# Kernel optimization log

Hardware: AMD Instinct MI355X
Metric: run time of the kernel (lower is better)

The kernel has to match this reference:

```python
import jax, jax.numpy as jnp
import numpy as np

T, B, H, D = 512, 64, 512, 32  # timesteps, batch, hidden_size, process_dim


def _softplus_beta(x, beta):
    # torch.nn.Softplus(beta): log(1+exp(beta*x))/beta
    return jax.nn.softplus(beta * x) / beta


def setup_inputs() -> dict:
    key = jax.random.key(0)
    ks = jax.random.split(key, 5)
    seq_dt = jax.random.uniform(ks[0], (T, B), jnp.float32)  # time until next event
    seq_types = jax.random.randint(ks[1], (T, B), 0, D)      # event type ids in [0, D)
    embed = jax.random.normal(ks[2], (D + 1, D), jnp.float32) * 0.1
    embed = embed.at[D].set(0.0)  # padding_idx row
    # 7 gate linears fused: order [input_g, forget_g, output_g, input_target, forget_target, z_gate, decay]
    W_gates = jax.random.normal(ks[3], (D + H, 7 * H), jnp.float32) * (1.0 / np.sqrt(D + H))
    b_gates = jax.random.normal(ks[4], (7 * H,), jnp.float32) * 0.05
    h0 = jnp.zeros((B, H), jnp.float32)
    c0 = jnp.zeros((B, H), jnp.float32)
    c_target0 = jnp.zeros((B, H), jnp.float32)
    return dict(seq_dt=seq_dt, seq_types=seq_types, embed=embed,
                W_gates=W_gates, b_gates=b_gates, h0=h0, c0=c0, c_target0=c_target0)


def reference(seq_dt, seq_types, embed, W_gates, b_gates, h0, c0, c_target0):
    def step(carry, inp):
        h, c, ctar = carry
        dt, types = inp
        x = embed[types]                       # (B, D) event embedding
        v = jnp.concatenate([x, h], axis=1)    # (B, D+H)
        g = v @ W_gates + b_gates              # (B, 7H) fused gate GEMM
        gi, gf, go, git, gft, gz, gd = jnp.split(g, 7, axis=1)
        inpt = jax.nn.sigmoid(gi)
        forget = jax.nn.sigmoid(gf)
        output = jax.nn.sigmoid(go)
        in_tar = jax.nn.sigmoid(git)
        fg_tar = jax.nn.sigmoid(gft)
        z = jnp.tanh(gz)
        decay = _softplus_beta(gd, 10.0)
        c_i = forget * c + inpt * z
        ctar_new = fg_tar * ctar + in_tar * z
        c_t = ctar_new + (c_i - ctar_new) * jnp.exp(-decay * dt[:, None])
        h_t = output * jnp.tanh(c_t)
        return (h_t, c_t, ctar_new), (h_t, output, c_i, ctar_new, decay)

    _, outs = jax.lax.scan(step, (h0, c0, c_target0), (seq_dt, seq_types))
    # (hiddens_ti, outputs, cells, cell_targets, decays), each (T, B, H)
    return outs
```

## Files before the change

### kernel.cpp

```cpp
#include <hip/hip_runtime.h>
#include <math.h>

#define T_ 512
#define B_ 64
#define H_ 512
#define D_ 32
#define G7H (7*H_)
#define NBLK 128
#define NTHR 512
#define JPB 4
#define BH (B_*H_)

typedef _Float16 f16x8 __attribute__((ext_vector_type(8)));
typedef float f32x4  __attribute__((ext_vector_type(4)));
typedef int   i32x2  __attribute__((ext_vector_type(2)));

__global__ void precompute_P2(const float* __restrict__ embed,
                              const float* __restrict__ Wg,
                              const float* __restrict__ bg,
                              float* __restrict__ P2) {
    int idx = blockIdx.x * blockDim.x + threadIdx.x;
    if (idx >= 33 * H_ * 8) return;
    int gate = idx & 7;
    int j    = (idx >> 3) & (H_ - 1);
    int type = idx >> 12;
    float acc = 0.f;
    if (gate < 7) {
        acc = bg[gate * H_ + j];
        #pragma unroll
        for (int d = 0; d < D_; ++d)
            acc += embed[type * D_ + d] * Wg[(size_t)d * G7H + gate * H_ + j];
    }
    P2[idx] = acc;
}

__global__ void precompute_Wt16(const float* __restrict__ Wg,
                                _Float16* __restrict__ Wt) {
    int idx = blockIdx.x * blockDim.x + threadIdx.x;
    if (idx >= G7H * H_) return;
    int k = idx & (H_ - 1);
    int n = idx >> 9;
    Wt[idx] = (_Float16)Wg[(size_t)(D_ + k) * G7H + n];
}

__global__ void init_h16(const float* __restrict__ h0, _Float16* __restrict__ hf) {
    int idx = blockIdx.x * blockDim.x + threadIdx.x;
    if (idx >= BH) return;
    hf[idx] = (_Float16)h0[idx];
}

__device__ __forceinline__ f16x8 load16_sc1(const _Float16* p) {
    f16x8 v;
    asm volatile("global_load_dwordx4 %0, %1, off sc1"
                 : "=v"(v) : "v"(p) : "memory");
    return v;
}

__device__ __forceinline__ float fast_rcp(float x) {
    float r;
    asm("v_rcp_f32 %0, %1" : "=v"(r) : "v"(x));
    return r;
}
__device__ __forceinline__ float fast_sigmoid(float x) {
    return fast_rcp(1.f + __expf(-x));
}
__device__ __forceinline__ float fast_tanh(float x) {
    return 1.f - 2.f * fast_rcp(1.f + __expf(2.f * x));
}

__global__ void __launch_bounds__(NTHR, 1)
hawkes_main(const float* __restrict__ seq_dt, const int* __restrict__ seq_types,
            const float* __restrict__ c0, const float* __restrict__ ct0,
            const float* __restrict__ P2,
            const _Float16* __restrict__ Wt,
            _Float16* __restrict__ hf,
            int* __restrict__ flags,
            float* __restrict__ out) {
    __shared__ f32x4 pcl[4][2][64];
    __shared__ float gl[B_][36];

    const int tid  = threadIdx.x;
    const int w    = tid >> 6;
    const int lane = tid & 63;
    const int wm   = w & 3;
    const int kh   = w >> 2;
    const int bid  = blockIdx.x;
    const int j0   = (bid & 7) * 64 + (bid >> 3) * JPB;
    const int m0   = wm * 16;

    f16x8 Bf[2][8];
    {
        const f16x8 zfrag = {0, 0, 0, 0, 0, 0, 0, 0};
        const int krow = (lane >> 4) << 3;
        #pragma unroll
        for (int nt = 0; nt < 2; ++nt) {
            const int c_local = nt * 16 + (lane & 15);
            const int gate = c_local & 7, jl2 = c_local >> 3;
            const bool pad = (gate == 7);
            const size_t nbase = pad ? 0 : (size_t)(gate * H_ + j0 + jl2) * (size_t)H_;
            #pragma unroll
            for (int kt = 0; kt < 8; ++kt) {
                const int k0 = kh * 256 + kt * 32 + krow;
                f16x8 v = *(const f16x8*)(Wt + nbase + k0);
                Bf[nt][kt] = pad ? zfrag : v;
            }
        }
    }

    const int eb = tid >> 2, ejl = tid & 3, ej = j0 + ejl;
    float c_s = 0.f, ct_s = 0.f;
    if (tid < 256) {
        c_s  = c0 [eb * H_ + ej];
        ct_s = ct0[eb * H_ + ej];
    }

    const size_t TBH = (size_t)T_ * BH;
    const int arow = m0 + (lane & 15);
    const int kb0  = kh * 256 + ((lane >> 4) << 3);

    for (int t = 0; t < T_; ++t) {
        int   type = 0; float dtv = 0.f;
        float4 pa = {0,0,0,0}, pb = {0,0,0,0};
        if (tid < 256) {
            type = seq_types[t * B_ + eb];
            dtv  = seq_dt  [t * B_ + eb];
            const float* pr = P2 + ((size_t)type * H_ + ej) * 8;
            pa = *(const float4*)pr;
            pb = *(const float4*)(pr + 4);
        }

        const _Float16* ph = hf + (t & 1) * BH + arow * H_ + kb0;

        f16x8 Af[8];
        #pragma unroll
        for (int kt = 0; kt < 8; ++kt) Af[kt] = load16_sc1(ph + kt * 32);
        asm volatile("s_waitcnt vmcnt(0)" ::: "memory");
        __builtin_amdgcn_sched_barrier(0);

        f32x4 acc0 = {0.f,0.f,0.f,0.f}, acc1 = {0.f,0.f,0.f,0.f};
        #pragma unroll
        for (int kt = 0; kt < 8; ++kt) {
            acc0 = __builtin_amdgcn_mfma_f32_16x16x32_f16(Af[kt], Bf[0][kt], acc0, 0, 0, 0);
            acc1 = __builtin_amdgcn_mfma_f32_16x16x32_f16(Af[kt], Bf[1][kt], acc1, 0, 0, 0);
        }

        if (kh == 1) { pcl[wm][0][lane] = acc0; pcl[wm][1][lane] = acc1; }
        __syncthreads();
        if (kh == 0) {
            f32x4 s0 = acc0 + pcl[wm][0][lane];
            f32x4 s1 = acc1 + pcl[wm][1][lane];
            const int col = lane & 15, rbase = m0 + ((lane >> 4) << 2);
            #pragma unroll
            for (int r = 0; r < 4; ++r) {
                gl[rbase + r][col]      = s0[r];
                gl[rbase + r][16 + col] = s1[r];
            }
        }
        __syncthreads();

        float h_t = 0.f, outp = 0.f, c_i = 0.f, ctar_new = 0.f, decay = 0.f;
        if (tid < 256) {
            const int b = eb;
            float4 ga = *(const float4*)&gl[b][ejl * 8];
            float4 gb = *(const float4*)&gl[b][ejl * 8 + 4];
            const float g0 = ga.x + pa.x, g1 = ga.y + pa.y, g2 = ga.z + pa.z, g3 = ga.w + pa.w;
            const float g4 = gb.x + pb.x, g5 = gb.y + pb.y, g6 = gb.z + pb.z;

            const float inpt   = fast_sigmoid(g0);
            const float forget = fast_sigmoid(g1);
            outp               = fast_sigmoid(g2);
            const float in_tar = fast_sigmoid(g3);
            const float fg_tar = fast_sigmoid(g4);
            const float z      = fast_tanh(g5);
            const float y      = 10.f * g6;
            decay              = (fmaxf(y, 0.f) + __logf(1.f + __expf(-fabsf(y)))) * 0.1f;

            c_i      = forget * c_s + inpt * z;
            ctar_new = fg_tar * ct_s + in_tar * z;
            const float c_t = ctar_new + (c_i - ctar_new) * __expf(-decay * dtv);
            h_t      = outp * fast_tanh(c_t);
            c_s  = c_t;
            ct_s = ctar_new;

            union { _Float16 f; unsigned short u; } cv; cv.f = (_Float16)h_t;
            unsigned hs = cv.u;
            unsigned oh = (unsigned)__shfl_down((int)hs, 1);
            if ((ejl & 1) == 0) {
                unsigned* dh = (unsigned*)(hf + ((t + 1) & 1) * BH) + ((eb * H_ + ej) >> 1);
                __hip_atomic_store(dh, hs | (oh << 16), __ATOMIC_RELAXED, __HIP_MEMORY_SCOPE_AGENT);
            }
        }

        __syncthreads();
        if (tid == 0)
            __hip_atomic_store(flags + bid, t + 1, __ATOMIC_RELAXED, __HIP_MEMORY_SCOPE_AGENT);

        if (tid < 256) {
            const size_t base = (size_t)t * BH + (size_t)eb * H_ + ej;
            out[base]           = h_t;
            out[TBH + base]     = outp;
            out[2 * TBH + base] = c_i;
            out[3 * TBH + base] = ctar_new;
            out[4 * TBH + base] = decay;
        }

        if (w == 0) {
            const int* fp = flags + 2 * lane;
            int ok;
            do {
                i32x2 vv;
                asm volatile("global_load_dwordx2 %0, %1, off sc1\n\t"
                             "s_waitcnt vmcnt(0)"
                             : "=&v"(vv) : "v"(fp) : "memory");
                ok = (vv.x >= t + 1) && (vv.y >= t + 1);
            } while (!__all(ok));
        }
        __syncthreads();
    }
}

extern "C" void kernel_launch(void* const* d_in, const int* in_sizes, int n_in,
                              void* d_out, int out_size, void* d_ws, size_t ws_size,
                              hipStream_t stream) {
    const float* seq_dt    = (const float*)d_in[0];
    const int*   seq_types = (const int*)  d_in[1];
    const float* embed     = (const float*)d_in[2];
    const float* W_gates   = (const float*)d_in[3];
    const float* b_gates   = (const float*)d_in[4];
    const float* h0        = (const float*)d_in[5];
    const float* c0        = (const float*)d_in[6];
    const float* ct0       = (const float*)d_in[7];
    float* out = (float*)d_out;

    float* P2 = (float*)d_ws;
    _Float16* Wt = (_Float16*)(P2 + 33 * H_ * 8);
    _Float16* hf = Wt + (size_t)G7H * H_;
    int* flags = (int*)(hf + 2 * BH);

    hipMemsetAsync(flags, 0, NBLK * sizeof(int), stream);
    {
        int total = 33 * H_ * 8;
        precompute_P2<<<(total + 255) / 256, 256, 0, stream>>>(embed, W_gates, b_gates, P2);
    }
    {
        int total = G7H * H_;
        precompute_Wt16<<<(total + 255) / 256, 256, 0, stream>>>(W_gates, Wt);
    }
    {
        int total = BH;
        init_h16<<<(total + 255) / 256, 256, 0, stream>>>(h0, hf);
    }
    {
        void* args[] = {(void*)&seq_dt, (void*)&seq_types, (void*)&c0, (void*)&ct0,
                        (void*)&P2, (void*)&Wt, (void*)&hf, (void*)&flags, (void*)&out};
        hipLaunchCooperativeKernel((void*)hawkes_main, dim3(NBLK), dim3(NTHR),
                                   args, 0, stream);
    }
}
```

Baseline: 2.039 ms.

## Move grid flag spin to step start and drop a per-step block barrier

Every wave now polls the cross-block progress flags itself at the start of each timestep. This replaces the single-wave poll at the end of the step and the block barrier that followed it. The gate reduction and the elementwise LSTM update are merged into one kh==0 section, which removes another __syncthreads. The five output values are staged in LDS and written to global memory after the flag is published, so those stores overlap the next step's wait. Weight fragment loads at setup become inline asm with immediate offsets. The trade-off is that all eight waves now spin on the flags, which adds extra polling traffic.

```diff
diff --git a/kernel.cpp b/kernel.cpp
--- a/kernel.cpp
+++ b/kernel.cpp
@@ -49,13 +49,6 @@
     hf[idx] = (_Float16)h0[idx];
 }
 
-__device__ __forceinline__ f16x8 load16_sc1(const _Float16* p) {
-    f16x8 v;
-    asm volatile("global_load_dwordx4 %0, %1, off sc1"
-                 : "=v"(v) : "v"(p) : "memory");
-    return v;
-}
-
 __device__ __forceinline__ float fast_rcp(float x) {
     float r;
     asm("v_rcp_f32 %0, %1" : "=v"(r) : "v"(x));
@@ -67,6 +60,13 @@
 __device__ __forceinline__ float fast_tanh(float x) {
     return 1.f - 2.f * fast_rcp(1.f + __expf(2.f * x));
 }
+
+#define LOADB(dst, p, OFF) \
+    asm volatile("global_load_dwordx4 %0, %1, off offset:" #OFF \
+                 : "=v"(dst) : "v"(p))
+#define LOADA(dst, p, OFF) \
+    asm volatile("global_load_dwordx4 %0, %1, off offset:" #OFF " sc1" \
+                 : "=v"(dst) : "v"(p) : "memory")
 
 __global__ void __launch_bounds__(NTHR, 1)
 hawkes_main(const float* __restrict__ seq_dt, const int* __restrict__ seq_types,
@@ -88,23 +88,35 @@
     const int j0   = (bid & 7) * 64 + (bid >> 3) * JPB;
     const int m0   = wm * 16;
 
+    const int  krow = (lane >> 4) << 3;
+    const bool pad  = (lane & 7) == 7;
+    const _Float16* wp0;
+    const _Float16* wp1;
+    {
+        const int gate = lane & 7;
+        const int jlA = ((lane & 15) >> 3);
+        const int jlB = 2 + ((lane & 15) >> 3);
+        wp0 = Wt + (pad ? 0 : (size_t)(gate * H_ + j0 + jlA) * (size_t)H_) + kh * 256 + krow;
+        wp1 = Wt + (pad ? 0 : (size_t)(gate * H_ + j0 + jlB) * (size_t)H_) + kh * 256 + krow;
+    }
+    f16x8 Br[2][8];
+    LOADB(Br[0][0], wp0, 0);   LOADB(Br[0][1], wp0, 64);
+    LOADB(Br[0][2], wp0, 128); LOADB(Br[0][3], wp0, 192);
+    LOADB(Br[0][4], wp0, 256); LOADB(Br[0][5], wp0, 320);
+    LOADB(Br[0][6], wp0, 384); LOADB(Br[0][7], wp0, 448);
+    LOADB(Br[1][0], wp1, 0);   LOADB(Br[1][1], wp1, 64);
+    LOADB(Br[1][2], wp1, 128); LOADB(Br[1][3], wp1, 192);
+    LOADB(Br[1][4], wp1, 256); LOADB(Br[1][5], wp1, 320);
+    LOADB(Br[1][6], wp1, 384); LOADB(Br[1][7], wp1, 448);
+    asm volatile("s_waitcnt vmcnt(0)" ::: "memory");
     f16x8 Bf[2][8];
     {
         const f16x8 zfrag = {0, 0, 0, 0, 0, 0, 0, 0};
-        const int krow = (lane >> 4) << 3;
         #pragma unroll
-        for (int nt = 0; nt < 2; ++nt) {
-            const int c_local = nt * 16 + (lane & 15);
-            const int gate = c_local & 7, jl2 = c_local >> 3;
-            const bool pad = (gate == 7);
-            const size_t nbase = pad ? 0 : (size_t)(gate * H_ + j0 + jl2) * (size_t)H_;
+        for (int nt = 0; nt < 2; ++nt)
             #pragma unroll
-            for (int kt = 0; kt < 8; ++kt) {
-                const int k0 = kh * 256 + kt * 32 + krow;
-                f16x8 v = *(const f16x8*)(Wt + nbase + k0);
-                Bf[nt][kt] = pad ? zfrag : v;
-            }
-        }
+            for (int kt = 0; kt < 8; ++kt)
+                Bf[nt][kt] = pad ? zfrag : Br[nt][kt];
     }
 
     const int eb = tid >> 2, ejl = tid & 3, ej = j0 + ejl;
@@ -116,7 +128,7 @@
 
     const size_t TBH = (size_t)T_ * BH;
     const int arow = m0 + (lane & 15);
-    const int kb0  = kh * 256 + ((lane >> 4) << 3);
+    const int kb0  = kh * 256 + krow;
 
     for (int t = 0; t < T_; ++t) {
         int   type = 0; float dtv = 0.f;
@@ -129,11 +141,24 @@
             pb = *(const float4*)(pr + 4);
         }
 
+        {
+            const int* fp = flags + 2 * lane;
+            int ok;
+            do {
+                i32x2 vv;
+                asm volatile("global_load_dwordx2 %0, %1, off sc1\n\t"
+                             "s_waitcnt vmcnt(0)"
+                             : "=&v"(vv) : "v"(fp) : "memory");
+                ok = (vv.x >= t) && (vv.y >= t);
+            } while (!__all(ok));
+        }
+
         const _Float16* ph = hf + (t & 1) * BH + arow * H_ + kb0;
-
         f16x8 Af[8];
-        #pragma unroll
-        for (int kt = 0; kt < 8; ++kt) Af[kt] = load16_sc1(ph + kt * 32);
+        LOADA(Af[0], ph, 0);   LOADA(Af[1], ph, 64);
+        LOADA(Af[2], ph, 128); LOADA(Af[3], ph, 192);
+        LOADA(Af[4], ph, 256); LOADA(Af[5], ph, 320);
+        LOADA(Af[6], ph, 384); LOADA(Af[7], ph, 448);
         asm volatile("s_waitcnt vmcnt(0)" ::: "memory");
         __builtin_amdgcn_sched_barrier(0);
 
@@ -146,6 +171,7 @@
 
         if (kh == 1) { pcl[wm][0][lane] = acc0; pcl[wm][1][lane] = acc1; }
         __syncthreads();
+
         if (kh == 0) {
             f32x4 s0 = acc0 + pcl[wm][0][lane];
             f32x4 s1 = acc1 + pcl[wm][1][lane];
@@ -155,30 +181,27 @@
                 gl[rbase + r][col]      = s0[r];
                 gl[rbase + r][16 + col] = s1[r];
             }
-        }
-        __syncthreads();
-
-        float h_t = 0.f, outp = 0.f, c_i = 0.f, ctar_new = 0.f, decay = 0.f;
-        if (tid < 256) {
-            const int b = eb;
-            float4 ga = *(const float4*)&gl[b][ejl * 8];
-            float4 gb = *(const float4*)&gl[b][ejl * 8 + 4];
+            asm volatile("s_waitcnt lgkmcnt(0)" ::: "memory");
+            __builtin_amdgcn_sched_barrier(0);
+
+            float4 ga = *(const float4*)&gl[eb][ejl * 8];
+            float4 gb = *(const float4*)&gl[eb][ejl * 8 + 4];
             const float g0 = ga.x + pa.x, g1 = ga.y + pa.y, g2 = ga.z + pa.z, g3 = ga.w + pa.w;
             const float g4 = gb.x + pb.x, g5 = gb.y + pb.y, g6 = gb.z + pb.z;
 
             const float inpt   = fast_sigmoid(g0);
             const float forget = fast_sigmoid(g1);
-            outp               = fast_sigmoid(g2);
+            const float outp   = fast_sigmoid(g2);
             const float in_tar = fast_sigmoid(g3);
             const float fg_tar = fast_sigmoid(g4);
             const float z      = fast_tanh(g5);
             const float y      = 10.f * g6;
-            decay              = (fmaxf(y, 0.f) + __logf(1.f + __expf(-fabsf(y)))) * 0.1f;
-
-            c_i      = forget * c_s + inpt * z;
-            ctar_new = fg_tar * ct_s + in_tar * z;
+            const float decay  = (fmaxf(y, 0.f) + __logf(1.f + __expf(-fabsf(y)))) * 0.1f;
+
+            const float c_i      = forget * c_s + inpt * z;
+            const float ctar_new = fg_tar * ct_s + in_tar * z;
             const float c_t = ctar_new + (c_i - ctar_new) * __expf(-decay * dtv);
-            h_t      = outp * fast_tanh(c_t);
+            const float h_t = outp * fast_tanh(c_t);
             c_s  = c_t;
             ct_s = ctar_new;
 
@@ -189,6 +212,12 @@
                 unsigned* dh = (unsigned*)(hf + ((t + 1) & 1) * BH) + ((eb * H_ + ej) >> 1);
                 __hip_atomic_store(dh, hs | (oh << 16), __ATOMIC_RELAXED, __HIP_MEMORY_SCOPE_AGENT);
             }
+
+            gl[eb][ejl * 8 + 0] = h_t;
+            gl[eb][ejl * 8 + 1] = outp;
+            gl[eb][ejl * 8 + 2] = c_i;
+            gl[eb][ejl * 8 + 3] = ctar_new;
+            gl[eb][ejl * 8 + 4] = decay;
         }
 
         __syncthreads();
@@ -197,25 +226,12 @@
 
         if (tid < 256) {
             const size_t base = (size_t)t * BH + (size_t)eb * H_ + ej;
-            out[base]           = h_t;
-            out[TBH + base]     = outp;
-            out[2 * TBH + base] = c_i;
-            out[3 * TBH + base] = ctar_new;
-            out[4 * TBH + base] = decay;
-        }
-
-        if (w == 0) {
-            const int* fp = flags + 2 * lane;
-            int ok;
-            do {
-                i32x2 vv;
-                asm volatile("global_load_dwordx2 %0, %1, off sc1\n\t"
-                             "s_waitcnt vmcnt(0)"
-                             : "=&v"(vv) : "v"(fp) : "memory");
-                ok = (vv.x >= t + 1) && (vv.y >= t + 1);
-            } while (!__all(ok));
-        }
-        __syncthreads();
+            out[base]           = gl[eb][ejl * 8 + 0];
+            out[TBH + base]     = gl[eb][ejl * 8 + 1];
+            out[2 * TBH + base] = gl[eb][ejl * 8 + 2];
+            out[3 * TBH + base] = gl[eb][ejl * 8 + 3];
+            out[4 * TBH + base] = gl[eb][ejl * 8 + 4];
+        }
     }
 }
 
```

After: 2.792 ms. 1.37x slower.

## Halve persistent grid to 64 blocks with 8 hidden units each and split-K reduction

Applied to the files above, without the earlier changes.

Reduces the cooperative grid from 128 to 64 blocks, so each block computes 8 hidden units using four MFMA N-tiles per wave. The two K-halves now each reduce half of the N-tiles, so all 512 threads run the elementwise gate math and one block barrier is removed. Next-step types, dt and P2 rows are prefetched before the cross-block flag wait, and the wait polls one flag per lane. Fewer blocks make the per-step grid barrier cheaper, at the cost of doubling MFMA and register work per block.

```diff
diff --git a/kernel.cpp b/kernel.cpp
--- a/kernel.cpp
+++ b/kernel.cpp
@@ -6,14 +6,13 @@
 #define H_ 512
 #define D_ 32
 #define G7H (7*H_)
-#define NBLK 128
+#define NBLK 64
 #define NTHR 512
-#define JPB 4
+#define JPB 8
 #define BH (B_*H_)
 
 typedef _Float16 f16x8 __attribute__((ext_vector_type(8)));
 typedef float f32x4  __attribute__((ext_vector_type(4)));
-typedef int   i32x2  __attribute__((ext_vector_type(2)));
 
 __global__ void precompute_P2(const float* __restrict__ embed,
                               const float* __restrict__ Wg,
@@ -49,13 +48,6 @@
     hf[idx] = (_Float16)h0[idx];
 }
 
-__device__ __forceinline__ f16x8 load16_sc1(const _Float16* p) {
-    f16x8 v;
-    asm volatile("global_load_dwordx4 %0, %1, off sc1"
-                 : "=v"(v) : "v"(p) : "memory");
-    return v;
-}
-
 __device__ __forceinline__ float fast_rcp(float x) {
     float r;
     asm("v_rcp_f32 %0, %1" : "=v"(r) : "v"(x));
@@ -67,6 +59,10 @@
 __device__ __forceinline__ float fast_tanh(float x) {
     return 1.f - 2.f * fast_rcp(1.f + __expf(2.f * x));
 }
+
+#define LOADA(dst, p, OFF) \
+    asm volatile("global_load_dwordx4 %0, %1, off offset:" #OFF " sc1" \
+                 : "=v"(dst) : "v"(p) : "memory")
 
 __global__ void __launch_bounds__(NTHR, 1)
 hawkes_main(const float* __restrict__ seq_dt, const int* __restrict__ seq_types,
@@ -76,8 +72,8 @@
             _Float16* __restrict__ hf,
             int* __restrict__ flags,
             float* __restrict__ out) {
-    __shared__ f32x4 pcl[4][2][64];
-    __shared__ float gl[B_][36];
+    __shared__ f32x4 pcl[4][4][64];
+    __shared__ float gl[B_][68];
 
     const int tid  = threadIdx.x;
     const int w    = tid >> 6;
@@ -87,116 +83,122 @@
     const int bid  = blockIdx.x;
     const int j0   = (bid & 7) * 64 + (bid >> 3) * JPB;
     const int m0   = wm * 16;
-
-    f16x8 Bf[2][8];
-    {
-        const f16x8 zfrag = {0, 0, 0, 0, 0, 0, 0, 0};
-        const int krow = (lane >> 4) << 3;
+    const int krow = (lane >> 4) << 3;
+
+    f16x8 Bf[4][8];
+    {
+        const f16x8 zf = {0, 0, 0, 0, 0, 0, 0, 0};
         #pragma unroll
-        for (int nt = 0; nt < 2; ++nt) {
-            const int c_local = nt * 16 + (lane & 15);
-            const int gate = c_local & 7, jl2 = c_local >> 3;
+        for (int nt = 0; nt < 4; ++nt) {
+            const int cl = nt * 16 + (lane & 15);
+            const int gate = cl & 7, jl2 = cl >> 3;
             const bool pad = (gate == 7);
-            const size_t nbase = pad ? 0 : (size_t)(gate * H_ + j0 + jl2) * (size_t)H_;
+            const size_t nb = pad ? 0 : (size_t)(gate * H_ + j0 + jl2) * (size_t)H_;
             #pragma unroll
             for (int kt = 0; kt < 8; ++kt) {
-                const int k0 = kh * 256 + kt * 32 + krow;
-                f16x8 v = *(const f16x8*)(Wt + nbase + k0);
-                Bf[nt][kt] = pad ? zfrag : v;
-            }
-        }
-    }
-
-    const int eb = tid >> 2, ejl = tid & 3, ej = j0 + ejl;
-    float c_s = 0.f, ct_s = 0.f;
-    if (tid < 256) {
-        c_s  = c0 [eb * H_ + ej];
-        ct_s = ct0[eb * H_ + ej];
+                f16x8 v = *(const f16x8*)(Wt + nb + kh * 256 + kt * 32 + krow);
+                Bf[nt][kt] = pad ? zf : v;
+            }
+        }
+    }
+
+    const int cb  = m0 + (lane & 15);
+    const int cjl = kh * 4 + (lane >> 4);
+    const int cj  = j0 + cjl;
+    float c_s  = c0 [cb * H_ + cj];
+    float ct_s = ct0[cb * H_ + cj];
+
+    int   typ = seq_types[cb];
+    float dtv = seq_dt[cb];
+    float4 pa, pb;
+    {
+        const float* pr = P2 + ((size_t)typ * H_ + cj) * 8;
+        pa = *(const float4*)pr;
+        pb = *(const float4*)(pr + 4);
     }
 
     const size_t TBH = (size_t)T_ * BH;
-    const int arow = m0 + (lane & 15);
-    const int kb0  = kh * 256 + ((lane >> 4) << 3);
+    const int kb0 = kh * 256 + krow;
 
     for (int t = 0; t < T_; ++t) {
-        int   type = 0; float dtv = 0.f;
-        float4 pa = {0,0,0,0}, pb = {0,0,0,0};
-        if (tid < 256) {
-            type = seq_types[t * B_ + eb];
-            dtv  = seq_dt  [t * B_ + eb];
-            const float* pr = P2 + ((size_t)type * H_ + ej) * 8;
-            pa = *(const float4*)pr;
-            pb = *(const float4*)(pr + 4);
-        }
-
-        const _Float16* ph = hf + (t & 1) * BH + arow * H_ + kb0;
-
+        const _Float16* ph = hf + (t & 1) * BH + cb * H_ + kb0;
         f16x8 Af[8];
-        #pragma unroll
-        for (int kt = 0; kt < 8; ++kt) Af[kt] = load16_sc1(ph + kt * 32);
+        LOADA(Af[0], ph, 0);   LOADA(Af[1], ph, 64);
+        LOADA(Af[2], ph, 128); LOADA(Af[3], ph, 192);
+        LOADA(Af[4], ph, 256); LOADA(Af[5], ph, 320);
+        LOADA(Af[6], ph, 384); LOADA(Af[7], ph, 448);
         asm volatile("s_waitcnt vmcnt(0)" ::: "memory");
         __builtin_amdgcn_sched_barrier(0);
 
-        f32x4 acc0 = {0.f,0.f,0.f,0.f}, acc1 = {0.f,0.f,0.f,0.f};
+        f32x4 a0 = {0.f,0.f,0.f,0.f}, a1 = {0.f,0.f,0.f,0.f};
+        f32x4 a2 = {0.f,0.f,0.f,0.f}, a3 = {0.f,0.f,0.f,0.f};
         #pragma unroll
         for (int kt = 0; kt < 8; ++kt) {
-            acc0 = __builtin_amdgcn_mfma_f32_16x16x32_f16(Af[kt], Bf[0][kt], acc0, 0, 0, 0);
-            acc1 = __builtin_amdgcn_mfma_f32_16x16x32_f16(Af[kt], Bf[1][kt], acc1, 0, 0, 0);
-        }
-
-        if (kh == 1) { pcl[wm][0][lane] = acc0; pcl[wm][1][lane] = acc1; }
-        __syncthreads();
-        if (kh == 0) {
-            f32x4 s0 = acc0 + pcl[wm][0][lane];
-            f32x4 s1 = acc1 + pcl[wm][1][lane];
-            const int col = lane & 15, rbase = m0 + ((lane >> 4) << 2);
+            a0 = __builtin_amdgcn_mfma_f32_16x16x32_f16(Af[kt], Bf[0][kt], a0, 0, 0, 0);
+            a1 = __builtin_amdgcn_mfma_f32_16x16x32_f16(Af[kt], Bf[1][kt], a1, 0, 0, 0);
+            a2 = __builtin_amdgcn_mfma_f32_16x16x32_f16(Af[kt], Bf[2][kt], a2, 0, 0, 0);
+            a3 = __builtin_amdgcn_mfma_f32_16x16x32_f16(Af[kt], Bf[3][kt], a3, 0, 0, 0);
+        }
+
+        if (kh == 0) { pcl[wm][2][lane] = a2; pcl[wm][3][lane] = a3; }
+        else         { pcl[wm][0][lane] = a0; pcl[wm][1][lane] = a1; }
+        asm volatile("s_waitcnt lgkmcnt(0)" ::: "memory");
+        __builtin_amdgcn_sched_barrier(0);
+        __builtin_amdgcn_s_barrier();
+
+        f32x4 sA, sB;
+        if (kh == 0) { sA = a0 + pcl[wm][0][lane]; sB = a1 + pcl[wm][1][lane]; }
+        else         { sA = a2 + pcl[wm][2][lane]; sB = a3 + pcl[wm][3][lane]; }
+
+        {
+            const int col = lane & 15, rb2 = m0 + ((lane >> 4) << 2), cbs = kh * 32;
             #pragma unroll
             for (int r = 0; r < 4; ++r) {
-                gl[rbase + r][col]      = s0[r];
-                gl[rbase + r][16 + col] = s1[r];
-            }
-        }
-        __syncthreads();
-
-        float h_t = 0.f, outp = 0.f, c_i = 0.f, ctar_new = 0.f, decay = 0.f;
-        if (tid < 256) {
-            const int b = eb;
-            float4 ga = *(const float4*)&gl[b][ejl * 8];
-            float4 gb = *(const float4*)&gl[b][ejl * 8 + 4];
-            const float g0 = ga.x + pa.x, g1 = ga.y + pa.y, g2 = ga.z + pa.z, g3 = ga.w + pa.w;
-            const float g4 = gb.x + pb.x, g5 = gb.y + pb.y, g6 = gb.z + pb.z;
-
-            const float inpt   = fast_sigmoid(g0);
-            const float forget = fast_sigmoid(g1);
-            outp               = fast_sigmoid(g2);
-            const float in_tar = fast_sigmoid(g3);
-            const float fg_tar = fast_sigmoid(g4);
-            const float z      = fast_tanh(g5);
-            const float y      = 10.f * g6;
-            decay              = (fmaxf(y, 0.f) + __logf(1.f + __expf(-fabsf(y)))) * 0.1f;
-
-            c_i      = forget * c_s + inpt * z;
-            ctar_new = fg_tar * ct_s + in_tar * z;
-            const float c_t = ctar_new + (c_i - ctar_new) * __expf(-decay * dtv);
-            h_t      = outp * fast_tanh(c_t);
-            c_s  = c_t;
-            ct_s = ctar_new;
-
+                gl[rb2 + r][cbs + col]      = sA[r];
+                gl[rb2 + r][cbs + 16 + col] = sB[r];
+            }
+        }
+        asm volatile("s_waitcnt lgkmcnt(0)" ::: "memory");
+        __builtin_amdgcn_sched_barrier(0);
+
+        float4 ga = *(const float4*)&gl[cb][cjl * 8];
+        float4 gb = *(const float4*)&gl[cb][cjl * 8 + 4];
+        const float g0 = ga.x + pa.x, g1 = ga.y + pa.y, g2 = ga.z + pa.z, g3 = ga.w + pa.w;
+        const float g4 = gb.x + pb.x, g5 = gb.y + pb.y, g6 = gb.z + pb.z;
+
+        const float inpt   = fast_sigmoid(g0);
+        const float forget = fast_sigmoid(g1);
+        const float outp   = fast_sigmoid(g2);
+        const float in_tar = fast_sigmoid(g3);
+        const float fg_tar = fast_sigmoid(g4);
+        const float z      = fast_tanh(g5);
+        const float y      = 10.f * g6;
+        const float decay  = (fmaxf(y, 0.f) + __logf(1.f + __expf(-fabsf(y)))) * 0.1f;
+
+        const float c_i      = forget * c_s + inpt * z;
+        const float ctar_new = fg_tar * ct_s + in_tar * z;
+        const float c_t = ctar_new + (c_i - ctar_new) * __expf(-decay * dtv);
+        const float h_t = outp * fast_tanh(c_t);
+        c_s  = c_t;
+        ct_s = ctar_new;
+
+        {
             union { _Float16 f; unsigned short u; } cv; cv.f = (_Float16)h_t;
             unsigned hs = cv.u;
-            unsigned oh = (unsigned)__shfl_down((int)hs, 1);
-            if ((ejl & 1) == 0) {
-                unsigned* dh = (unsigned*)(hf + ((t + 1) & 1) * BH) + ((eb * H_ + ej) >> 1);
+            unsigned oh = (unsigned)__shfl_down((int)hs, 16);
+            if (((lane >> 4) & 1) == 0) {
+                unsigned* dh = (unsigned*)(hf + ((t + 1) & 1) * BH) + ((cb * H_ + cj) >> 1);
                 __hip_atomic_store(dh, hs | (oh << 16), __ATOMIC_RELAXED, __HIP_MEMORY_SCOPE_AGENT);
             }
         }
-
-        __syncthreads();
+        asm volatile("s_waitcnt vmcnt(0)" ::: "memory");
+        __builtin_amdgcn_sched_barrier(0);
+        __builtin_amdgcn_s_barrier();
         if (tid == 0)
             __hip_atomic_store(flags + bid, t + 1, __ATOMIC_RELAXED, __HIP_MEMORY_SCOPE_AGENT);
 
-        if (tid < 256) {
-            const size_t base = (size_t)t * BH + (size_t)eb * H_ + ej;
+        {
+            const size_t base = (size_t)t * BH + (size_t)cb * H_ + cj;
             out[base]           = h_t;
             out[TBH + base]     = outp;
             out[2 * TBH + base] = c_i;
@@ -204,18 +206,30 @@
             out[4 * TBH + base] = decay;
         }
 
-        if (w == 0) {
-            const int* fp = flags + 2 * lane;
-            int ok;
-            do {
-                i32x2 vv;
-                asm volatile("global_load_dwordx2 %0, %1, off sc1\n\t"
-                             "s_waitcnt vmcnt(0)"
-                             : "=&v"(vv) : "v"(fp) : "memory");
-                ok = (vv.x >= t + 1) && (vv.y >= t + 1);
-            } while (!__all(ok));
-        }
-        __syncthreads();
+        {
+            const int tn = (t + 1 < T_) ? t + 1 : t;
+            typ = seq_types[tn * B_ + cb];
+            dtv = seq_dt  [tn * B_ + cb];
+            const float* pr = P2 + ((size_t)typ * H_ + cj) * 8;
+            pa = *(const float4*)pr;
+            pb = *(const float4*)(pr + 4);
+        }
+
+        if (t + 1 < T_) {
+            if (w == 0) {
+                const int* fp = flags + lane;
+                int ok;
+                do {
+                    int v;
+                    asm volatile("global_load_dword %0, %1, off sc1\n\t"
+                                 "s_waitcnt vmcnt(0)"
+                                 : "=&v"(v) : "v"(fp) : "memory");
+                    ok = v >= t + 1;
+                } while (!__all(ok));
+            }
+            __builtin_amdgcn_sched_barrier(0);
+            __builtin_amdgcn_s_barrier();
+        }
     }
 }
 
@@ -237,7 +251,7 @@
     _Float16* hf = Wt + (size_t)G7H * H_;
     int* flags = (int*)(hf + 2 * BH);
 
-    hipMemsetAsync(flags, 0, NBLK * sizeof(int), stream);
+    hipMemsetAsync(flags, 0, 256 * sizeof(int), stream);
     {
         int total = 33 * H_ * 8;
         precompute_P2<<<(total + 255) / 256, 256, 0, stream>>>(embed, W_gates, b_gates, P2);
```

Result: slower. 2.631 ms (+29.1%).
